# Kernel optimization log

Hardware: AMD Instinct MI355X
Metric: run time of the kernel (lower is better)

The kernel has to match this reference:

```python
import jax, jax.numpy as jnp
import numpy as np

H = 512          # hidden_size
L = 1024         # total sequence length (q_len + c_len + t_len)
C = 512          # number of columns (key/value length)
NUM_REL = 51     # len(relations2id)


def setup_inputs() -> dict:
    key = jax.random.key(0)
    ks = jax.random.split(key, 12)
    w = 1.0 / np.sqrt(H)  # torch nn.Linear default init scale
    return {
        "query": jax.random.normal(ks[0], (1, L, H), jnp.float32),
        "key": jax.random.normal(ks[1], (1, C, H), jnp.float32),
        "value": jax.random.normal(ks[2], (1, C, H), jnp.float32),
        "predefined_relation": jax.random.randint(ks[3], (L, L), 0, NUM_REL, dtype=jnp.int32),
        "q_len": 384,
        "c_len": 512,
        "Wq": jax.random.uniform(ks[4], (H, H), jnp.float32, -w, w),
        "bq": jnp.zeros((H,), jnp.float32),
        "Wk": jax.random.uniform(ks[5], (H, H), jnp.float32, -w, w),
        "bk": jnp.zeros((H,), jnp.float32),
        "Wv": jax.random.uniform(ks[6], (H, H), jnp.float32, -w, w),
        "bv": jnp.zeros((H,), jnp.float32),
        "rel_k_emb": jax.random.normal(ks[7], (NUM_REL, H), jnp.float32),
        "rel_v_emb": jax.random.normal(ks[8], (NUM_REL, H), jnp.float32),
    }


def reference(query, key, value, predefined_relation, q_len, c_len,
              Wq, bq, Wk, bk, Wv, bv, rel_k_emb, rel_v_emb):
    # --- get_fixed_column_relation (kind='column', enable_latent_relations=False) ---
    # predefined_relation: [L, L] relation ids; take column block [L, C]
    mc = predefined_relation[:, q_len:q_len + c_len]          # [L, C]
    relation_k = rel_k_emb[mc]                                # [L, C, H]
    relation_v = rel_v_emb[mc]                                # [L, C, H] (value path discarded by forward)
    # --- single-head projections (nbatches == 1) ---
    q = query[0] @ Wq.T + bq                                  # [L, H]
    k = key[0] @ Wk.T + bk                                    # [C, H]
    v = value[0] @ Wv.T + bv                                  # [C, H]
    # --- relative_attention_logits ---
    qk = q @ k.T                                              # [L, C]
    q_rel = jnp.einsum('lh,lch->lc', q, relation_k)           # per-query relation scores [L, C]
    scores = (qk + q_rel) / np.sqrt(H).astype(np.float32)
    attn = jax.nn.softmax(scores, axis=-1)                    # [L, C]
    # forward returns self.attn[0, 0] (the pre-dropout attention probabilities);
    # relative_attention_values output (attn @ v + einsum('lc,lch->lh', attn, relation_v))
    # is computed in the torch module but discarded, so we return only attn.
    return attn
```

## Files before the change

### kernel.cpp

```cpp
#include <hip/hip_runtime.h>
#include <hip/hip_bf16.h>

#define HH 512
#define LL 1024
#define CC 512
#define NREL 51

typedef __attribute__((ext_vector_type(8))) short bf16x8;
typedef __attribute__((ext_vector_type(4))) float f32x4;

__device__ __forceinline__ short f2bn(float f) {
    return __builtin_bit_cast(short, __float2bfloat16(f));
}

__device__ __forceinline__ void gl16(const void* g, void* l) {
    __builtin_amdgcn_global_load_lds(
        (const __attribute__((address_space(1))) void*)g,
        (__attribute__((address_space(3))) void*)l, 16, 0, 0);
}

__global__ __launch_bounds__(256) void k0_prep(
    const float* __restrict__ query, const float* __restrict__ key,
    const float* __restrict__ Wq, const float* __restrict__ Wk,
    const float* __restrict__ relk,
    short* __restrict__ queryb, short* __restrict__ keyb,
    short* __restrict__ Wqb, short* __restrict__ Wkb, short* __restrict__ relkb,
    float* __restrict__ Rbuf)
{
    const int z = blockIdx.x * 256 + threadIdx.x;
    const float4 zz = make_float4(0.f, 0.f, 0.f, 0.f);
    if (z < 16384) ((float4*)Rbuf)[z] = zz;
    if (z < 832)  ((float4*)(relkb + 51 * HH))[z] = zz;
    for (int u = blockIdx.x * 256 + threadIdx.x; u < 167104; u += 131072) {
        const float* src; short* dst; int c;
        if (u < 65536)       { src = query; dst = queryb; c = u; }
        else if (u < 98304)  { src = key;   dst = keyb;   c = u - 65536; }
        else if (u < 131072) { src = Wq;    dst = Wqb;    c = u - 98304; }
        else if (u < 163840) { src = Wk;    dst = Wkb;    c = u - 131072; }
        else                 { src = relk;  dst = relkb;  c = u - 163840; }
        float4 x = *(const float4*)(src + c * 8);
        float4 y = *(const float4*)(src + c * 8 + 4);
        bf16x8 o;
        o[0] = f2bn(x.x); o[1] = f2bn(x.y); o[2] = f2bn(x.z); o[3] = f2bn(x.w);
        o[4] = f2bn(y.x); o[5] = f2bn(y.y); o[6] = f2bn(y.z); o[7] = f2bn(y.w);
        const int cs = c ^ ((c >> 6) & 7);
        *(bf16x8*)(dst + cs * 8) = o;
    }
}

__global__ __launch_bounds__(64) void k1_proj(
    const short* __restrict__ queryb, const short* __restrict__ keyb,
    const short* __restrict__ Wqb, const short* __restrict__ Wkb,
    const short* __restrict__ relkb, const float* __restrict__ bq,
    short* __restrict__ qbuf, short* __restrict__ kbuf,
    float* __restrict__ Rbuf)
{
    __shared__ __align__(16) short buf[2][5120];
    __shared__ __align__(16) short rl[5120];
    const int b = blockIdx.x, l = threadIdx.x;
    const bool isq = (b < 512);
    const short *A, *B; short* outp; int m0, n0;
    if (isq) { A = queryb; B = Wqb; outp = qbuf;
               m0 = (b >> 3) * 16; n0 = (b & 7) * 64; }
    else     { const int bb = b - 512; A = keyb; B = Wkb; outp = kbuf;
               m0 = (bb >> 3) * 16; n0 = (bb & 7) * 64; }
    const int lr = l & 15, lk = (l >> 4) * 8;
    const int lx = 8 * (lr & 7);
    const int srow = l >> 3, scol = (l & 7) * 8;

    if (isq) {
        #pragma unroll
        for (int j = 0; j < 8; ++j)
            gl16(relkb + (j * 8 + srow) * HH + n0 + scol, rl + j * 512);
    }

#define K1_STAGE(bi, t) do { \
        const int k0 = (t) * 64; \
        short* Lb = buf[bi]; \
        _Pragma("unroll") \
        for (int j = 0; j < 2; ++j) \
            gl16(A + (m0 + j * 8 + srow) * HH + k0 + scol, Lb + j * 512); \
        _Pragma("unroll") \
        for (int j = 0; j < 8; ++j) \
            gl16(B + (n0 + j * 8 + srow) * HH + k0 + scol, Lb + 1024 + j * 512); \
    } while (0)

    f32x4 acc[4] = {};
#define K1_COMP(bi) do { \
        const short* Lb = buf[bi]; \
        bf16x8 a0 = *(const bf16x8*)(Lb + lr * 64 + ((0 + lk) ^ lx)); \
        bf16x8 a1 = *(const bf16x8*)(Lb + lr * 64 + ((32 + lk) ^ lx)); \
        _Pragma("unroll") \
        for (int f = 0; f < 4; ++f) { \
            bf16x8 b0 = *(const bf16x8*)(Lb + 1024 + (f * 16 + lr) * 64 + ((0 + lk) ^ lx)); \
            bf16x8 b1 = *(const bf16x8*)(Lb + 1024 + (f * 16 + lr) * 64 + ((32 + lk) ^ lx)); \
            acc[f] = __builtin_amdgcn_mfma_f32_16x16x32_bf16(a0, b0, acc[f], 0, 0, 0); \
            acc[f] = __builtin_amdgcn_mfma_f32_16x16x32_bf16(a1, b1, acc[f], 0, 0, 0); \
        } \
    } while (0)

    K1_STAGE(0, 0);
    #pragma unroll
    for (int t = 0; t < 8; ++t) {
        if (t < 7) {
            K1_STAGE((t + 1) & 1, t + 1);
            asm volatile("s_waitcnt vmcnt(10)" ::: "memory");
        } else {
            asm volatile("s_waitcnt vmcnt(0)" ::: "memory");
        }
        __builtin_amdgcn_sched_barrier(0);
        K1_COMP(t & 1);
    }
#undef K1_STAGE
#undef K1_COMP

    if (isq) {
        short* qt = rl + 4096;
        #pragma unroll
        for (int f = 0; f < 4; ++f) {
            const int colg = f * 16 + lr;
            const float bv = bq[n0 + colg];
            #pragma unroll
            for (int r = 0; r < 4; ++r) {
                const int row = (l >> 4) * 4 + r;
                const short h = f2bn(acc[f][r] + bv);
                outp[(m0 + row) * HH + n0 + (colg ^ (8 * (row & 7)))] = h;
                qt[row * 64 + (((colg >> 3) ^ (row & 7)) << 3) + (colg & 7)] = h;
            }
        }
        f32x4 racc[4] = {};
        bf16x8 a0 = *(const bf16x8*)(qt + lr * 64 + ((0 + lk) ^ lx));
        bf16x8 a1 = *(const bf16x8*)(qt + lr * 64 + ((32 + lk) ^ lx));
        #pragma unroll
        for (int f = 0; f < 4; ++f) {
            bf16x8 b0 = *(const bf16x8*)(rl + (f * 16 + lr) * 64 + ((0 + lk) ^ lx));
            bf16x8 b1 = *(const bf16x8*)(rl + (f * 16 + lr) * 64 + ((32 + lk) ^ lx));
            racc[f] = __builtin_amdgcn_mfma_f32_16x16x32_bf16(a0, b0, racc[f], 0, 0, 0);
            racc[f] = __builtin_amdgcn_mfma_f32_16x16x32_bf16(a1, b1, racc[f], 0, 0, 0);
        }
        #pragma unroll
        for (int f = 0; f < 4; ++f)
            #pragma unroll
            for (int r = 0; r < 4; ++r)
                atomicAdd(Rbuf + (m0 + (l >> 4) * 4 + r) * 64 + f * 16 + lr,
                          racc[f][r]);
    } else {
        #pragma unroll
        for (int f = 0; f < 4; ++f) {
            const int colg = f * 16 + lr;
            #pragma unroll
            for (int r = 0; r < 4; ++r) {
                const int row = m0 + (l >> 4) * 4 + r;
                outp[row * HH + n0 + (colg ^ (8 * (row & 7)))] = f2bn(acc[f][r]);
            }
        }
    }
}

__global__ __launch_bounds__(64) void k2_attn(
    const short* __restrict__ qbuf, const short* __restrict__ kbuf,
    const int* __restrict__ rel, const int* __restrict__ qlen,
    const float* __restrict__ Rbuf, float* __restrict__ Ssum,
    float* __restrict__ out)
{
    __shared__ __align__(16) short buf[3][5120];
    const int b = blockIdx.x, l = threadIdx.x;
    const int l0 = (b >> 3) * 16, cg = b & 7, cb = cg * 64;
    const int lr = l & 15, lk = (l >> 4) * 8;
    const int lx = 8 * (lr & 7);
    const int srow = l >> 3, scol = (l & 7) * 8;
    const int qoff = qlen[0];

    int idxr[4][4];
    #pragma unroll
    for (int r = 0; r < 4; ++r) {
        const int row = (l >> 4) * 4 + r;
        #pragma unroll
        for (int f = 0; f < 4; ++f)
            idxr[r][f] = rel[(l0 + row) * LL + qoff + cb + f * 16 + lr];
    }

#define K2_STAGE(bi, t) do { \
        const int k0 = (t) * 64; \
        short* Lb = buf[bi]; \
        _Pragma("unroll") \
        for (int j = 0; j < 2; ++j) \
            gl16(qbuf + (l0 + j * 8 + srow) * HH + k0 + scol, Lb + j * 512); \
        _Pragma("unroll") \
        for (int j = 0; j < 8; ++j) \
            gl16(kbuf + (cb + j * 8 + srow) * HH + k0 + scol, Lb + 1024 + j * 512); \
    } while (0)

    f32x4 acc[4] = {};
#define K2_COMP(bi) do { \
        const short* Lb = buf[bi]; \
        bf16x8 a0 = *(const bf16x8*)(Lb + lr * 64 + ((0 + lk) ^ lx)); \
        bf16x8 a1 = *(const bf16x8*)(Lb + lr * 64 + ((32 + lk) ^ lx)); \
        _Pragma("unroll") \
        for (int f = 0; f < 4; ++f) { \
            const int ro = (f * 16 + lr) * 64; \
            bf16x8 k0v = *(const bf16x8*)(Lb + 1024 + ro + ((0 + lk) ^ lx)); \
            bf16x8 k1v = *(const bf16x8*)(Lb + 1024 + ro + ((32 + lk) ^ lx)); \
            acc[f] = __builtin_amdgcn_mfma_f32_16x16x32_bf16(a0, k0v, acc[f], 0, 0, 0); \
            acc[f] = __builtin_amdgcn_mfma_f32_16x16x32_bf16(a1, k1v, acc[f], 0, 0, 0); \
        } \
    } while (0)

    float rv[4][4];
    K2_STAGE(0, 0); K2_STAGE(1, 1);
    #pragma unroll
    for (int t = 0; t < 8; ++t) {
        if (t < 6) {
            K2_STAGE((t + 2) % 3, t + 2);
            asm volatile("s_waitcnt vmcnt(20)" ::: "memory");
        } else if (t == 6) {
            asm volatile("s_waitcnt vmcnt(10)" ::: "memory");
            #pragma unroll
            for (int r = 0; r < 4; ++r)
                #pragma unroll
                for (int f = 0; f < 4; ++f)
                    rv[r][f] = Rbuf[(l0 + (l >> 4) * 4 + r) * 64 + idxr[r][f]];
        } else {
            asm volatile("s_waitcnt vmcnt(0)" ::: "memory");
        }
        __builtin_amdgcn_sched_barrier(0);
        K2_COMP(t % 3);
    }
#undef K2_STAGE
#undef K2_COMP

    const float scale = 0.04419417382415922f;
    #pragma unroll
    for (int r = 0; r < 4; ++r) {
        const int row = (l >> 4) * 4 + r;
        float s = 0.f;
        #pragma unroll
        for (int f = 0; f < 4; ++f) {
            float e = __expf((acc[f][r] + rv[r][f]) * scale);
            acc[f][r] = e; s += e;
        }
        #pragma unroll
        for (int sh = 1; sh < 16; sh <<= 1) s += __shfl_xor(s, sh, 64);
        if (lr == 0) Ssum[(l0 + row) * 8 + cg] = s;
    }
    #pragma unroll
    for (int f = 0; f < 4; ++f)
        #pragma unroll
        for (int r = 0; r < 4; ++r) {
            const int row = (l >> 4) * 4 + r;
            out[(l0 + row) * CC + cb + f * 16 + lr] = acc[f][r];
        }
}

__global__ __launch_bounds__(256) void k3_norm(
    const float* __restrict__ Ssum, float* __restrict__ out)
{
    const int e = (blockIdx.x * 256 + threadIdx.x) * 4;
    const int row = e >> 9;
    float4 s0 = *(const float4*)(Ssum + row * 8);
    float4 s1 = *(const float4*)(Ssum + row * 8 + 4);
    const float inv = 1.f / (s0.x + s0.y + s0.z + s0.w + s1.x + s1.y + s1.z + s1.w);
    float4 v = *(float4*)(out + e);
    v.x *= inv; v.y *= inv; v.z *= inv; v.w *= inv;
    *(float4*)(out + e) = v;
}

extern "C" void kernel_launch(void* const* d_in, const int* in_sizes, int n_in,
                              void* d_out, int out_size, void* d_ws, size_t ws_size,
                              hipStream_t stream) {
    const float* query = (const float*)d_in[0];
    const float* key   = (const float*)d_in[1];
    const int*   rel   = (const int*)d_in[3];
    const int*   qlen  = (const int*)d_in[4];
    const float* Wq    = (const float*)d_in[6];
    const float* bq    = (const float*)d_in[7];
    const float* Wk    = (const float*)d_in[8];
    const float* relk  = (const float*)d_in[12];

    float* out = (float*)d_out;
    short* p = (short*)d_ws;
    short* queryb = p;  p += LL * HH;
    short* keyb   = p;  p += CC * HH;
    short* Wqb    = p;  p += HH * HH;
    short* Wkb    = p;  p += HH * HH;
    short* relkb  = p;  p += 64 * HH;
    short* qbuf   = p;  p += LL * HH;
    short* kbuf   = p;  p += CC * HH;
    float* Ssum   = (float*)p;
    float* Rbuf   = Ssum + LL * 8;

    k0_prep<<<512, 256, 0, stream>>>(query, key, Wq, Wk, relk,
                                     queryb, keyb, Wqb, Wkb, relkb, Rbuf);
    k1_proj<<<768, 64, 0, stream>>>(queryb, keyb, Wqb, Wkb, relkb, bq,
                                    qbuf, kbuf, Rbuf);
    k2_attn<<<512, 64, 0, stream>>>(qbuf, kbuf, rel, qlen, Rbuf, Ssum, out);
    k3_norm<<<512, 256, 0, stream>>>(Ssum, out);
}
```

Baseline: 25.84 us.

## Split k2 attention K-dimension across four waves with LDS reduction

```diff
diff --git a/kernel.cpp b/kernel.cpp
--- a/kernel.cpp
+++ b/kernel.cpp
@@ -157,99 +157,121 @@
     }
 }
 
-__global__ __launch_bounds__(64) void k2_attn(
+__global__ __launch_bounds__(256) void k2_attn(
     const short* __restrict__ qbuf, const short* __restrict__ kbuf,
     const int* __restrict__ rel, const int* __restrict__ qlen,
     const float* __restrict__ Rbuf, float* __restrict__ Ssum,
     float* __restrict__ out)
 {
-    __shared__ __align__(16) short buf[3][5120];
+    __shared__ __align__(16) short buf[4][2][5120];
     const int b = blockIdx.x, l = threadIdx.x;
+    const int w = l >> 6, lane = l & 63;
     const int l0 = (b >> 3) * 16, cg = b & 7, cb = cg * 64;
-    const int lr = l & 15, lk = (l >> 4) * 8;
+    const int lr = lane & 15, lk = (lane >> 4) * 8;
     const int lx = 8 * (lr & 7);
-    const int srow = l >> 3, scol = (l & 7) * 8;
-    const int qoff = qlen[0];
+    const int srow = lane >> 3, scol = (lane & 7) * 8;
 
     int idxr[4][4];
-    #pragma unroll
-    for (int r = 0; r < 4; ++r) {
-        const int row = (l >> 4) * 4 + r;
-        #pragma unroll
-        for (int f = 0; f < 4; ++f)
-            idxr[r][f] = rel[(l0 + row) * LL + qoff + cb + f * 16 + lr];
-    }
-
-#define K2_STAGE(bi, t) do { \
+    float rv[4][4];
+    if (w == 0) {
+        const int qoff = qlen[0];
+        #pragma unroll
+        for (int r = 0; r < 4; ++r) {
+            const int row = (lane >> 4) * 4 + r;
+            #pragma unroll
+            for (int f = 0; f < 4; ++f)
+                idxr[r][f] = rel[(l0 + row) * LL + qoff + cb + f * 16 + lr];
+        }
+    }
+
+#define K2_STAGE(Lb, t) do { \
         const int k0 = (t) * 64; \
-        short* Lb = buf[bi]; \
         _Pragma("unroll") \
         for (int j = 0; j < 2; ++j) \
-            gl16(qbuf + (l0 + j * 8 + srow) * HH + k0 + scol, Lb + j * 512); \
+            gl16(qbuf + (l0 + j * 8 + srow) * HH + k0 + scol, (Lb) + j * 512); \
         _Pragma("unroll") \
         for (int j = 0; j < 8; ++j) \
-            gl16(kbuf + (cb + j * 8 + srow) * HH + k0 + scol, Lb + 1024 + j * 512); \
+            gl16(kbuf + (cb + j * 8 + srow) * HH + k0 + scol, (Lb) + 1024 + j * 512); \
     } while (0)
 
     f32x4 acc[4] = {};
-#define K2_COMP(bi) do { \
-        const short* Lb = buf[bi]; \
-        bf16x8 a0 = *(const bf16x8*)(Lb + lr * 64 + ((0 + lk) ^ lx)); \
-        bf16x8 a1 = *(const bf16x8*)(Lb + lr * 64 + ((32 + lk) ^ lx)); \
+#define K2_COMP(Lb) do { \
+        bf16x8 a0 = *(const bf16x8*)((Lb) + lr * 64 + ((0 + lk) ^ lx)); \
+        bf16x8 a1 = *(const bf16x8*)((Lb) + lr * 64 + ((32 + lk) ^ lx)); \
         _Pragma("unroll") \
         for (int f = 0; f < 4; ++f) { \
             const int ro = (f * 16 + lr) * 64; \
-            bf16x8 k0v = *(const bf16x8*)(Lb + 1024 + ro + ((0 + lk) ^ lx)); \
-            bf16x8 k1v = *(const bf16x8*)(Lb + 1024 + ro + ((32 + lk) ^ lx)); \
+            bf16x8 k0v = *(const bf16x8*)((Lb) + 1024 + ro + ((0 + lk) ^ lx)); \
+            bf16x8 k1v = *(const bf16x8*)((Lb) + 1024 + ro + ((32 + lk) ^ lx)); \
             acc[f] = __builtin_amdgcn_mfma_f32_16x16x32_bf16(a0, k0v, acc[f], 0, 0, 0); \
             acc[f] = __builtin_amdgcn_mfma_f32_16x16x32_bf16(a1, k1v, acc[f], 0, 0, 0); \
         } \
     } while (0)
 
-    float rv[4][4];
-    K2_STAGE(0, 0); K2_STAGE(1, 1);
-    #pragma unroll
-    for (int t = 0; t < 8; ++t) {
-        if (t < 6) {
-            K2_STAGE((t + 2) % 3, t + 2);
-            asm volatile("s_waitcnt vmcnt(20)" ::: "memory");
-        } else if (t == 6) {
-            asm volatile("s_waitcnt vmcnt(10)" ::: "memory");
-            #pragma unroll
-            for (int r = 0; r < 4; ++r)
-                #pragma unroll
-                for (int f = 0; f < 4; ++f)
-                    rv[r][f] = Rbuf[(l0 + (l >> 4) * 4 + r) * 64 + idxr[r][f]];
-        } else {
-            asm volatile("s_waitcnt vmcnt(0)" ::: "memory");
-        }
-        __builtin_amdgcn_sched_barrier(0);
-        K2_COMP(t % 3);
-    }
+    K2_STAGE(buf[w][0], 2 * w);
+    K2_STAGE(buf[w][1], 2 * w + 1);
+
+    if (w == 0) {
+        asm volatile("s_waitcnt vmcnt(20)" ::: "memory");
+        #pragma unroll
+        for (int r = 0; r < 4; ++r)
+            #pragma unroll
+            for (int f = 0; f < 4; ++f)
+                rv[r][f] = Rbuf[(l0 + (lane >> 4) * 4 + r) * 64 + idxr[r][f]];
+        asm volatile("s_waitcnt vmcnt(26)" ::: "memory");
+    } else {
+        asm volatile("s_waitcnt vmcnt(10)" ::: "memory");
+    }
+    __builtin_amdgcn_sched_barrier(0);
+    K2_COMP(buf[w][0]);
+    if (w == 0) {
+        asm volatile("s_waitcnt vmcnt(16)" ::: "memory");
+    } else {
+        asm volatile("s_waitcnt vmcnt(0)" ::: "memory");
+    }
+    __builtin_amdgcn_sched_barrier(0);
+    K2_COMP(buf[w][1]);
 #undef K2_STAGE
 #undef K2_COMP
 
-    const float scale = 0.04419417382415922f;
-    #pragma unroll
-    for (int r = 0; r < 4; ++r) {
-        const int row = (l >> 4) * 4 + r;
-        float s = 0.f;
-        #pragma unroll
-        for (int f = 0; f < 4; ++f) {
-            float e = __expf((acc[f][r] + rv[r][f]) * scale);
-            acc[f][r] = e; s += e;
-        }
-        #pragma unroll
-        for (int sh = 1; sh < 16; sh <<= 1) s += __shfl_xor(s, sh, 64);
-        if (lr == 0) Ssum[(l0 + row) * 8 + cg] = s;
-    }
-    #pragma unroll
-    for (int f = 0; f < 4; ++f)
+    if (w != 0) {
+        float* P = (float*)buf[w][0];
+        #pragma unroll
+        for (int f = 0; f < 4; ++f)
+            *(f32x4*)(P + lane * 16 + f * 4) = acc[f];
+    }
+    __syncthreads();
+
+    if (w == 0) {
+        #pragma unroll
+        for (int wv = 1; wv < 4; ++wv) {
+            const float* P = (const float*)buf[wv][0];
+            #pragma unroll
+            for (int f = 0; f < 4; ++f)
+                acc[f] += *(const f32x4*)(P + lane * 16 + f * 4);
+        }
+        const float scale = 0.04419417382415922f;
         #pragma unroll
         for (int r = 0; r < 4; ++r) {
-            const int row = (l >> 4) * 4 + r;
-            out[(l0 + row) * CC + cb + f * 16 + lr] = acc[f][r];
-        }
+            const int row = (lane >> 4) * 4 + r;
+            float s = 0.f;
+            #pragma unroll
+            for (int f = 0; f < 4; ++f) {
+                float e = __expf((acc[f][r] + rv[r][f]) * scale);
+                acc[f][r] = e; s += e;
+            }
+            #pragma unroll
+            for (int sh = 1; sh < 16; sh <<= 1) s += __shfl_xor(s, sh, 64);
+            if (lr == 0) Ssum[(l0 + row) * 8 + cg] = s;
+        }
+        #pragma unroll
+        for (int f = 0; f < 4; ++f)
+            #pragma unroll
+            for (int r = 0; r < 4; ++r) {
+                const int row = (lane >> 4) * 4 + r;
+                out[(l0 + row) * CC + cb + f * 16 + lr] = acc[f][r];
+            }
+    }
 }
 
 __global__ __launch_bounds__(256) void k3_norm(
@@ -293,6 +315,6 @@
                                      queryb, keyb, Wqb, Wkb, relkb, Rbuf);
     k1_proj<<<768, 64, 0, stream>>>(queryb, keyb, Wqb, Wkb, relkb, bq,
                                     qbuf, kbuf, Rbuf);
-    k2_attn<<<512, 64, 0, stream>>>(qbuf, kbuf, rel, qlen, Rbuf, Ssum, out);
+    k2_attn<<<512, 256, 0, stream>>>(qbuf, kbuf, rel, qlen, Rbuf, Ssum, out);
     k3_norm<<<512, 256, 0, stream>>>(Ssum, out);
 }
```

After: 26.39 us. +2.1%, slower.

## Fuse bf16 conversion into projection and softmax normalization into attention kernel

Applied to the files above, without the earlier changes.

```diff
diff --git a/kernel.cpp b/kernel.cpp
--- a/kernel.cpp
+++ b/kernel.cpp
@@ -8,6 +8,7 @@
 
 typedef __attribute__((ext_vector_type(8))) short bf16x8;
 typedef __attribute__((ext_vector_type(4))) float f32x4;
+typedef __attribute__((ext_vector_type(2))) float f32x2;
 
 __device__ __forceinline__ short f2bn(float f) {
     return __builtin_bit_cast(short, __float2bfloat16(f));
@@ -19,250 +20,238 @@
         (__attribute__((address_space(3))) void*)l, 16, 0, 0);
 }
 
-__global__ __launch_bounds__(256) void k0_prep(
+__global__ __launch_bounds__(256) void k1_proj(
     const float* __restrict__ query, const float* __restrict__ key,
     const float* __restrict__ Wq, const float* __restrict__ Wk,
-    const float* __restrict__ relk,
-    short* __restrict__ queryb, short* __restrict__ keyb,
-    short* __restrict__ Wqb, short* __restrict__ Wkb, short* __restrict__ relkb,
-    float* __restrict__ Rbuf)
+    const float* __restrict__ relk, const float* __restrict__ bq,
+    short* __restrict__ qbuf, short* __restrict__ kbuf,
+    float* __restrict__ Rpart)
 {
-    const int z = blockIdx.x * 256 + threadIdx.x;
-    const float4 zz = make_float4(0.f, 0.f, 0.f, 0.f);
-    if (z < 16384) ((float4*)Rbuf)[z] = zz;
-    if (z < 832)  ((float4*)(relkb + 51 * HH))[z] = zz;
-    for (int u = blockIdx.x * 256 + threadIdx.x; u < 167104; u += 131072) {
-        const float* src; short* dst; int c;
-        if (u < 65536)       { src = query; dst = queryb; c = u; }
-        else if (u < 98304)  { src = key;   dst = keyb;   c = u - 65536; }
-        else if (u < 131072) { src = Wq;    dst = Wqb;    c = u - 98304; }
-        else if (u < 163840) { src = Wk;    dst = Wkb;    c = u - 131072; }
-        else                 { src = relk;  dst = relkb;  c = u - 163840; }
-        float4 x = *(const float4*)(src + c * 8);
-        float4 y = *(const float4*)(src + c * 8 + 4);
-        bf16x8 o;
-        o[0] = f2bn(x.x); o[1] = f2bn(x.y); o[2] = f2bn(x.z); o[3] = f2bn(x.w);
-        o[4] = f2bn(y.x); o[5] = f2bn(y.y); o[6] = f2bn(y.z); o[7] = f2bn(y.w);
-        const int cs = c ^ ((c >> 6) & 7);
-        *(bf16x8*)(dst + cs * 8) = o;
-    }
-}
-
-__global__ __launch_bounds__(64) void k1_proj(
-    const short* __restrict__ queryb, const short* __restrict__ keyb,
-    const short* __restrict__ Wqb, const short* __restrict__ Wkb,
-    const short* __restrict__ relkb, const float* __restrict__ bq,
-    short* __restrict__ qbuf, short* __restrict__ kbuf,
-    float* __restrict__ Rbuf)
+    __shared__ __align__(16) short Alds[16 * 512];
+    __shared__ __align__(16) short Blds[64 * 512];
+    const int b = blockIdx.x, tid = threadIdx.x;
+    const int w = tid >> 6, lane = tid & 63;
+    const bool isq = (b < 512);
+    const float *A, *B; short* outp; int m0, n0;
+    if (isq) { A = query; B = Wq; outp = qbuf;
+               m0 = (b >> 3) * 16; n0 = (b & 7) * 64; }
+    else     { const int bb = b - 512; A = key; B = Wk; outp = kbuf;
+               m0 = (bb >> 3) * 16; n0 = (bb & 7) * 64; }
+
+    {
+        const int ar = tid >> 4, ac = (tid & 15) * 8;
+        #pragma unroll
+        for (int j = 0; j < 4; ++j) {
+            const int c = ac + j * 128;
+            float4 x = *(const float4*)(A + (m0 + ar) * HH + c);
+            float4 y = *(const float4*)(A + (m0 + ar) * HH + c + 4);
+            bf16x8 o;
+            o[0] = f2bn(x.x); o[1] = f2bn(x.y); o[2] = f2bn(x.z); o[3] = f2bn(x.w);
+            o[4] = f2bn(y.x); o[5] = f2bn(y.y); o[6] = f2bn(y.z); o[7] = f2bn(y.w);
+            *(bf16x8*)(Alds + ar * 512 + (((c >> 3) ^ (ar & 7)) << 3)) = o;
+        }
+        const int br = tid >> 2, bc = (tid & 3) * 16;
+        #pragma unroll
+        for (int j = 0; j < 8; ++j) {
+            const int c = bc + j * 64;
+            float4 x0 = *(const float4*)(B + (n0 + br) * HH + c);
+            float4 x1 = *(const float4*)(B + (n0 + br) * HH + c + 4);
+            float4 x2 = *(const float4*)(B + (n0 + br) * HH + c + 8);
+            float4 x3 = *(const float4*)(B + (n0 + br) * HH + c + 12);
+            bf16x8 o0, o1;
+            o0[0] = f2bn(x0.x); o0[1] = f2bn(x0.y); o0[2] = f2bn(x0.z); o0[3] = f2bn(x0.w);
+            o0[4] = f2bn(x1.x); o0[5] = f2bn(x1.y); o0[6] = f2bn(x1.z); o0[7] = f2bn(x1.w);
+            o1[0] = f2bn(x2.x); o1[1] = f2bn(x2.y); o1[2] = f2bn(x2.z); o1[3] = f2bn(x2.w);
+            o1[4] = f2bn(x3.x); o1[5] = f2bn(x3.y); o1[6] = f2bn(x3.z); o1[7] = f2bn(x3.w);
+            *(bf16x8*)(Blds + br * 512 + ((((c >> 3) + 0) ^ (br & 7)) << 3)) = o0;
+            *(bf16x8*)(Blds + br * 512 + ((((c >> 3) + 1) ^ (br & 7)) << 3)) = o1;
+        }
+    }
+    __syncthreads();
+
+    const int lr = lane & 15, lk = (lane >> 4) * 8;
+    const int lx = 8 * (lr & 7);
+    f32x4 acc[4] = {};
+    #pragma unroll
+    for (int t = 0; t < 2; ++t) {
+        const int k0g = w * 128 + t * 64;
+        bf16x8 a0 = *(const bf16x8*)(Alds + lr * 512 + k0g + ((0 + lk) ^ lx));
+        bf16x8 a1 = *(const bf16x8*)(Alds + lr * 512 + k0g + ((32 + lk) ^ lx));
+        #pragma unroll
+        for (int f = 0; f < 4; ++f) {
+            const int ro = (f * 16 + lr) * 512 + k0g;
+            bf16x8 b0 = *(const bf16x8*)(Blds + ro + ((0 + lk) ^ lx));
+            bf16x8 b1 = *(const bf16x8*)(Blds + ro + ((32 + lk) ^ lx));
+            acc[f] = __builtin_amdgcn_mfma_f32_16x16x32_bf16(a0, b0, acc[f], 0, 0, 0);
+            acc[f] = __builtin_amdgcn_mfma_f32_16x16x32_bf16(a1, b1, acc[f], 0, 0, 0);
+        }
+    }
+    __syncthreads();
+
+    float* P = (float*)Blds;
+    if (w) {
+        #pragma unroll
+        for (int f = 0; f < 4; ++f)
+            *(f32x4*)(P + (w - 1) * 1024 + lane * 16 + f * 4) = acc[f];
+    }
+    __syncthreads();
+
+    short* qt   = Blds + 8192;
+    short* Brel = Blds + 16384;
+    if (w == 0) {
+        #pragma unroll
+        for (int wv = 0; wv < 3; ++wv)
+            #pragma unroll
+            for (int f = 0; f < 4; ++f)
+                acc[f] += *(const f32x4*)(P + wv * 1024 + lane * 16 + f * 4);
+        #pragma unroll
+        for (int f = 0; f < 4; ++f) {
+            const int colg = f * 16 + lr;
+            const float bv = isq ? bq[n0 + colg] : 0.f;
+            #pragma unroll
+            for (int r = 0; r < 4; ++r) {
+                const int row = (lane >> 4) * 4 + r;
+                const short h = f2bn(acc[f][r] + bv);
+                outp[(m0 + row) * HH + n0 + (colg ^ (8 * (row & 7)))] = h;
+                if (isq)
+                    qt[row * 64 + (((colg >> 3) ^ (row & 7)) << 3) + (colg & 7)] = h;
+            }
+        }
+    } else if (isq) {
+        for (int i = tid - 64; i < 1024; i += 192) {
+            const int rr = i >> 4, c4 = (i & 15) * 4;
+            float4 v = make_float4(0.f, 0.f, 0.f, 0.f);
+            if (rr < NREL) v = *(const float4*)(relk + rr * HH + n0 + c4);
+            short4 o;
+            o.x = f2bn(v.x); o.y = f2bn(v.y); o.z = f2bn(v.z); o.w = f2bn(v.w);
+            *(short4*)(Brel + rr * 64 + (((c4 >> 3) ^ (rr & 7)) << 3) + (c4 & 7)) = o;
+        }
+    }
+    __syncthreads();
+
+    if (w == 0 && isq) {
+        bf16x8 a0 = *(const bf16x8*)(qt + lr * 64 + ((0 + lk) ^ lx));
+        bf16x8 a1 = *(const bf16x8*)(qt + lr * 64 + ((32 + lk) ^ lx));
+        f32x4 racc[4] = {};
+        #pragma unroll
+        for (int f = 0; f < 4; ++f) {
+            const int ro = (f * 16 + lr) * 64;
+            bf16x8 b0 = *(const bf16x8*)(Brel + ro + ((0 + lk) ^ lx));
+            bf16x8 b1 = *(const bf16x8*)(Brel + ro + ((32 + lk) ^ lx));
+            racc[f] = __builtin_amdgcn_mfma_f32_16x16x32_bf16(a0, b0, racc[f], 0, 0, 0);
+            racc[f] = __builtin_amdgcn_mfma_f32_16x16x32_bf16(a1, b1, racc[f], 0, 0, 0);
+        }
+        #pragma unroll
+        for (int f = 0; f < 4; ++f)
+            #pragma unroll
+            for (int r = 0; r < 4; ++r)
+                Rpart[(b & 7) * (LL * 64) + (m0 + (lane >> 4) * 4 + r) * 64 + f * 16 + lr]
+                    = racc[f][r];
+    }
+}
+
+__global__ __launch_bounds__(512) void k2_attn(
+    const short* __restrict__ qbuf, const short* __restrict__ kbuf,
+    const int* __restrict__ rel, const int* __restrict__ qlen,
+    const float* __restrict__ Rpart, float* __restrict__ out)
 {
-    __shared__ __align__(16) short buf[2][5120];
-    __shared__ __align__(16) short rl[5120];
-    const int b = blockIdx.x, l = threadIdx.x;
-    const bool isq = (b < 512);
-    const short *A, *B; short* outp; int m0, n0;
-    if (isq) { A = queryb; B = Wqb; outp = qbuf;
-               m0 = (b >> 3) * 16; n0 = (b & 7) * 64; }
-    else     { const int bb = b - 512; A = keyb; B = Wkb; outp = kbuf;
-               m0 = (bb >> 3) * 16; n0 = (bb & 7) * 64; }
-    const int lr = l & 15, lk = (l >> 4) * 8;
+    __shared__ __align__(16) short Bb[8][2][4096];
+    __shared__ float Rs[16][64];
+    __shared__ float psum[8][16];
+    const int b = blockIdx.x, tid = threadIdx.x;
+    const int w = tid >> 6, lane = tid & 63;
+    const int l0 = b * 16, cb = w * 64;
+    const int lr = lane & 15, lk = (lane >> 4) * 8;
     const int lx = 8 * (lr & 7);
-    const int srow = l >> 3, scol = (l & 7) * 8;
-
-    if (isq) {
-        #pragma unroll
-        for (int j = 0; j < 8; ++j)
-            gl16(relkb + (j * 8 + srow) * HH + n0 + scol, rl + j * 512);
-    }
-
-#define K1_STAGE(bi, t) do { \
-        const int k0 = (t) * 64; \
-        short* Lb = buf[bi]; \
-        _Pragma("unroll") \
-        for (int j = 0; j < 2; ++j) \
-            gl16(A + (m0 + j * 8 + srow) * HH + k0 + scol, Lb + j * 512); \
+    const int srow = lane >> 3, scol = (lane & 7) * 8;
+    const int qoff = qlen[0];
+
+    const int rrow = tid >> 5, rc = (tid & 31) * 2;
+    f32x2 rpv[8];
+    #pragma unroll
+    for (int p = 0; p < 8; ++p)
+        rpv[p] = *(const f32x2*)(Rpart + p * (LL * 64) + (l0 + rrow) * 64 + rc);
+    int idxr[4][4];
+    #pragma unroll
+    for (int r = 0; r < 4; ++r) {
+        const int row = (lane >> 4) * 4 + r;
+        #pragma unroll
+        for (int f = 0; f < 4; ++f)
+            idxr[r][f] = rel[(l0 + row) * LL + qoff + cb + f * 16 + lr];
+    }
+    __builtin_amdgcn_sched_barrier(0);
+
+    bf16x8 a0v[2], a1v[2];
+#define K2_STAGE(bi, t) do { \
+        const int k0g = (t) * 64; \
+        short* Lb = &Bb[w][bi][0]; \
         _Pragma("unroll") \
         for (int j = 0; j < 8; ++j) \
-            gl16(B + (n0 + j * 8 + srow) * HH + k0 + scol, Lb + 1024 + j * 512); \
+            gl16(kbuf + (cb + j * 8 + srow) * HH + k0g + scol, Lb + j * 512); \
+        a0v[bi] = *(const bf16x8*)(qbuf + (l0 + lr) * HH + k0g + ((0 + lk) ^ lx)); \
+        a1v[bi] = *(const bf16x8*)(qbuf + (l0 + lr) * HH + k0g + ((32 + lk) ^ lx)); \
     } while (0)
 
     f32x4 acc[4] = {};
-#define K1_COMP(bi) do { \
-        const short* Lb = buf[bi]; \
-        bf16x8 a0 = *(const bf16x8*)(Lb + lr * 64 + ((0 + lk) ^ lx)); \
-        bf16x8 a1 = *(const bf16x8*)(Lb + lr * 64 + ((32 + lk) ^ lx)); \
+#define K2_COMP(bi) do { \
+        const short* Lb = &Bb[w][bi][0]; \
         _Pragma("unroll") \
         for (int f = 0; f < 4; ++f) { \
-            bf16x8 b0 = *(const bf16x8*)(Lb + 1024 + (f * 16 + lr) * 64 + ((0 + lk) ^ lx)); \
-            bf16x8 b1 = *(const bf16x8*)(Lb + 1024 + (f * 16 + lr) * 64 + ((32 + lk) ^ lx)); \
-            acc[f] = __builtin_amdgcn_mfma_f32_16x16x32_bf16(a0, b0, acc[f], 0, 0, 0); \
-            acc[f] = __builtin_amdgcn_mfma_f32_16x16x32_bf16(a1, b1, acc[f], 0, 0, 0); \
+            const int ro = (f * 16 + lr) * 64; \
+            bf16x8 k0f = *(const bf16x8*)(Lb + ro + ((0 + lk) ^ lx)); \
+            bf16x8 k1f = *(const bf16x8*)(Lb + ro + ((32 + lk) ^ lx)); \
+            acc[f] = __builtin_amdgcn_mfma_f32_16x16x32_bf16(a0v[bi], k0f, acc[f], 0, 0, 0); \
+            acc[f] = __builtin_amdgcn_mfma_f32_16x16x32_bf16(a1v[bi], k1f, acc[f], 0, 0, 0); \
         } \
     } while (0)
 
-    K1_STAGE(0, 0);
+    K2_STAGE(0, 0);
     #pragma unroll
     for (int t = 0; t < 8; ++t) {
         if (t < 7) {
-            K1_STAGE((t + 1) & 1, t + 1);
+            K2_STAGE((t + 1) & 1, t + 1);
             asm volatile("s_waitcnt vmcnt(10)" ::: "memory");
         } else {
             asm volatile("s_waitcnt vmcnt(0)" ::: "memory");
         }
         __builtin_amdgcn_sched_barrier(0);
-        K1_COMP(t & 1);
-    }
-#undef K1_STAGE
-#undef K1_COMP
-
-    if (isq) {
-        short* qt = rl + 4096;
-        #pragma unroll
-        for (int f = 0; f < 4; ++f) {
-            const int colg = f * 16 + lr;
-            const float bv = bq[n0 + colg];
-            #pragma unroll
-            for (int r = 0; r < 4; ++r) {
-                const int row = (l >> 4) * 4 + r;
-                const short h = f2bn(acc[f][r] + bv);
-                outp[(m0 + row) * HH + n0 + (colg ^ (8 * (row & 7)))] = h;
-                qt[row * 64 + (((colg >> 3) ^ (row & 7)) << 3) + (colg & 7)] = h;
-            }
-        }
-        f32x4 racc[4] = {};
-        bf16x8 a0 = *(const bf16x8*)(qt + lr * 64 + ((0 + lk) ^ lx));
-        bf16x8 a1 = *(const bf16x8*)(qt + lr * 64 + ((32 + lk) ^ lx));
-        #pragma unroll
-        for (int f = 0; f < 4; ++f) {
-            bf16x8 b0 = *(const bf16x8*)(rl + (f * 16 + lr) * 64 + ((0 + lk) ^ lx));
-            bf16x8 b1 = *(const bf16x8*)(rl + (f * 16 + lr) * 64 + ((32 + lk) ^ lx));
-            racc[f] = __builtin_amdgcn_mfma_f32_16x16x32_bf16(a0, b0, racc[f], 0, 0, 0);
-            racc[f] = __builtin_amdgcn_mfma_f32_16x16x32_bf16(a1, b1, racc[f], 0, 0, 0);
-        }
-        #pragma unroll
-        for (int f = 0; f < 4; ++f)
-            #pragma unroll
-            for (int r = 0; r < 4; ++r)
-                atomicAdd(Rbuf + (m0 + (l >> 4) * 4 + r) * 64 + f * 16 + lr,
-                          racc[f][r]);
-    } else {
-        #pragma unroll
-        for (int f = 0; f < 4; ++f) {
-            const int colg = f * 16 + lr;
-            #pragma unroll
-            for (int r = 0; r < 4; ++r) {
-                const int row = m0 + (l >> 4) * 4 + r;
-                outp[row * HH + n0 + (colg ^ (8 * (row & 7)))] = f2bn(acc[f][r]);
-            }
-        }
-    }
-}
-
-__global__ __launch_bounds__(64) void k2_attn(
-    const short* __restrict__ qbuf, const short* __restrict__ kbuf,
-    const int* __restrict__ rel, const int* __restrict__ qlen,
-    const float* __restrict__ Rbuf, float* __restrict__ Ssum,
-    float* __restrict__ out)
-{
-    __shared__ __align__(16) short buf[3][5120];
-    const int b = blockIdx.x, l = threadIdx.x;
-    const int l0 = (b >> 3) * 16, cg = b & 7, cb = cg * 64;
-    const int lr = l & 15, lk = (l >> 4) * 8;
-    const int lx = 8 * (lr & 7);
-    const int srow = l >> 3, scol = (l & 7) * 8;
-    const int qoff = qlen[0];
-
-    int idxr[4][4];
-    #pragma unroll
-    for (int r = 0; r < 4; ++r) {
-        const int row = (l >> 4) * 4 + r;
-        #pragma unroll
-        for (int f = 0; f < 4; ++f)
-            idxr[r][f] = rel[(l0 + row) * LL + qoff + cb + f * 16 + lr];
-    }
-
-#define K2_STAGE(bi, t) do { \
-        const int k0 = (t) * 64; \
-        short* Lb = buf[bi]; \
-        _Pragma("unroll") \
-        for (int j = 0; j < 2; ++j) \
-            gl16(qbuf + (l0 + j * 8 + srow) * HH + k0 + scol, Lb + j * 512); \
-        _Pragma("unroll") \
-        for (int j = 0; j < 8; ++j) \
-            gl16(kbuf + (cb + j * 8 + srow) * HH + k0 + scol, Lb + 1024 + j * 512); \
-    } while (0)
-
-    f32x4 acc[4] = {};
-#define K2_COMP(bi) do { \
-        const short* Lb = buf[bi]; \
-        bf16x8 a0 = *(const bf16x8*)(Lb + lr * 64 + ((0 + lk) ^ lx)); \
-        bf16x8 a1 = *(const bf16x8*)(Lb + lr * 64 + ((32 + lk) ^ lx)); \
-        _Pragma("unroll") \
-        for (int f = 0; f < 4; ++f) { \
-            const int ro = (f * 16 + lr) * 64; \
-            bf16x8 k0v = *(const bf16x8*)(Lb + 1024 + ro + ((0 + lk) ^ lx)); \
-            bf16x8 k1v = *(const bf16x8*)(Lb + 1024 + ro + ((32 + lk) ^ lx)); \
-            acc[f] = __builtin_amdgcn_mfma_f32_16x16x32_bf16(a0, k0v, acc[f], 0, 0, 0); \
-            acc[f] = __builtin_amdgcn_mfma_f32_16x16x32_bf16(a1, k1v, acc[f], 0, 0, 0); \
-        } \
-    } while (0)
-
-    float rv[4][4];
-    K2_STAGE(0, 0); K2_STAGE(1, 1);
-    #pragma unroll
-    for (int t = 0; t < 8; ++t) {
-        if (t < 6) {
-            K2_STAGE((t + 2) % 3, t + 2);
-            asm volatile("s_waitcnt vmcnt(20)" ::: "memory");
-        } else if (t == 6) {
-            asm volatile("s_waitcnt vmcnt(10)" ::: "memory");
-            #pragma unroll
-            for (int r = 0; r < 4; ++r)
-                #pragma unroll
-                for (int f = 0; f < 4; ++f)
-                    rv[r][f] = Rbuf[(l0 + (l >> 4) * 4 + r) * 64 + idxr[r][f]];
-        } else {
-            asm volatile("s_waitcnt vmcnt(0)" ::: "memory");
-        }
-        __builtin_amdgcn_sched_barrier(0);
-        K2_COMP(t % 3);
+        K2_COMP(t & 1);
     }
 #undef K2_STAGE
 #undef K2_COMP
 
+    float rx = 0.f, ry = 0.f;
+    #pragma unroll
+    for (int p = 0; p < 8; ++p) { rx += rpv[p][0]; ry += rpv[p][1]; }
+    Rs[rrow][rc] = rx; Rs[rrow][rc + 1] = ry;
+    __syncthreads();
+
     const float scale = 0.04419417382415922f;
     #pragma unroll
     for (int r = 0; r < 4; ++r) {
-        const int row = (l >> 4) * 4 + r;
+        const int row = (lane >> 4) * 4 + r;
         float s = 0.f;
         #pragma unroll
         for (int f = 0; f < 4; ++f) {
-            float e = __expf((acc[f][r] + rv[r][f]) * scale);
+            float e = __expf((acc[f][r] + Rs[row][idxr[r][f]]) * scale);
             acc[f][r] = e; s += e;
         }
         #pragma unroll
         for (int sh = 1; sh < 16; sh <<= 1) s += __shfl_xor(s, sh, 64);
-        if (lr == 0) Ssum[(l0 + row) * 8 + cg] = s;
-    }
-    #pragma unroll
-    for (int f = 0; f < 4; ++f)
-        #pragma unroll
-        for (int r = 0; r < 4; ++r) {
-            const int row = (l >> 4) * 4 + r;
-            out[(l0 + row) * CC + cb + f * 16 + lr] = acc[f][r];
-        }
-}
-
-__global__ __launch_bounds__(256) void k3_norm(
-    const float* __restrict__ Ssum, float* __restrict__ out)
-{
-    const int e = (blockIdx.x * 256 + threadIdx.x) * 4;
-    const int row = e >> 9;
-    float4 s0 = *(const float4*)(Ssum + row * 8);
-    float4 s1 = *(const float4*)(Ssum + row * 8 + 4);
-    const float inv = 1.f / (s0.x + s0.y + s0.z + s0.w + s1.x + s1.y + s1.z + s1.w);
-    float4 v = *(float4*)(out + e);
-    v.x *= inv; v.y *= inv; v.z *= inv; v.w *= inv;
-    *(float4*)(out + e) = v;
+        if (lr == 0) psum[w][row] = s;
+    }
+    __syncthreads();
+    #pragma unroll
+    for (int r = 0; r < 4; ++r) {
+        const int row = (lane >> 4) * 4 + r;
+        float tot = 0.f;
+        #pragma unroll
+        for (int wv = 0; wv < 8; ++wv) tot += psum[wv][row];
+        const float inv = 1.f / tot;
+        #pragma unroll
+        for (int f = 0; f < 4; ++f)
+            out[(l0 + row) * CC + cb + f * 16 + lr] = acc[f][r] * inv;
+    }
 }
 
 extern "C" void kernel_launch(void* const* d_in, const int* in_sizes, int n_in,
@@ -279,20 +268,11 @@
 
     float* out = (float*)d_out;
     short* p = (short*)d_ws;
-    short* queryb = p;  p += LL * HH;
-    short* keyb   = p;  p += CC * HH;
-    short* Wqb    = p;  p += HH * HH;
-    short* Wkb    = p;  p += HH * HH;
-    short* relkb  = p;  p += 64 * HH;
-    short* qbuf   = p;  p += LL * HH;
-    short* kbuf   = p;  p += CC * HH;
-    float* Ssum   = (float*)p;
-    float* Rbuf   = Ssum + LL * 8;
-
-    k0_prep<<<512, 256, 0, stream>>>(query, key, Wq, Wk, relk,
-                                     queryb, keyb, Wqb, Wkb, relkb, Rbuf);
-    k1_proj<<<768, 64, 0, stream>>>(queryb, keyb, Wqb, Wkb, relkb, bq,
-                                    qbuf, kbuf, Rbuf);
-    k2_attn<<<512, 64, 0, stream>>>(qbuf, kbuf, rel, qlen, Rbuf, Ssum, out);
-    k3_norm<<<512, 256, 0, stream>>>(Ssum, out);
-}
+    short* qbuf  = p;  p += LL * HH;
+    short* kbuf  = p;  p += CC * HH;
+    float* Rpart = (float*)p;
+
+    k1_proj<<<768, 256, 0, stream>>>(query, key, Wq, Wk, relk, bq,
+                                     qbuf, kbuf, Rpart);
+    k2_attn<<<64, 512, 0, stream>>>(qbuf, kbuf, rel, qlen, Rpart, out);
+}
```

Result: slower. 27.75 us (+7.4%).
